# Optimization experiments

Measured on AMD Instinct MI355X. Metric: run time of the kernel, lower is better.

Reference implementation:

```python
import jax, jax.numpy as jnp
import numpy as np

B, CIN, COUT, T, H, W, NH = 8, 16, 16, 32, 16, 16, 4
DIN = CIN * H * W    # 4096
DOUT = COUT * H * W  # 4096
DH = DOUT // NH      # 1024


def conv3d(x, w, b, pad):
    y = jax.lax.conv_general_dilated(
        x, w, window_strides=(1, 1, 1), padding=((pad, pad),) * 3,
        dimension_numbers=('NCDHW', 'OIDHW', 'NCDHW'))
    return y + b[None, :, None, None, None]


def instance_norm(x, eps=1e-5):
    # InstanceNorm3d default: no affine, normalize per (B,C) over (T,H,W)
    mu = x.mean(axis=(2, 3, 4), keepdims=True)
    var = ((x - mu) ** 2).mean(axis=(2, 3, 4), keepdims=True)
    return (x - mu) * jax.lax.rsqrt(var + eps)


def slstm(x, Wg, bg, Rg):
    # x: (B,T,D). Wg: (4,D,D) input weights [i,f,z,o]; bg: (4,D);
    # Rg: (NH,4,DH,DH) block-diagonal per-head recurrent weights.
    Bb, Tt, D = x.shape
    Gx = jnp.einsum('btd,god->btgo', x, Wg) + bg  # (B,T,4,D)

    def step(carry, gx):
        h, c, n, m = carry
        hh = h.reshape(Bb, NH, DH)
        gh = jnp.einsum('bhd,hgod->bhgo', hh, Rg)          # (B,NH,4,DH)
        pre = gx + gh.transpose(0, 2, 1, 3).reshape(Bb, 4, D)
        i_pre, f_pre, z_pre, o_pre = pre[:, 0], pre[:, 1], pre[:, 2], pre[:, 3]
        # stabilized exponential gating (xLSTM sLSTM)
        m_new = jnp.maximum(f_pre + m, i_pre)
        i = jnp.exp(i_pre - m_new)
        f = jnp.exp(f_pre + m - m_new)
        c = f * c + i * jnp.tanh(z_pre)
        n = f * n + i
        h = jax.nn.sigmoid(o_pre) * c / n
        return (h, c, n, m_new), h

    init = tuple(jnp.zeros((Bb, D), x.dtype) for _ in range(4))
    _, hs = jax.lax.scan(step, init, Gx.transpose(1, 0, 2, 3))  # hs: (T,B,D)
    return hs.transpose(1, 0, 2)


def setup_inputs():
    key = jax.random.key(0)
    ks = jax.random.split(key, 8)
    s = 0.02
    return {
        'x': jax.random.normal(ks[0], (B, CIN, T, H, W), jnp.float32),
        'c1_w': jax.random.normal(ks[1], (COUT, CIN, 3, 3, 3), jnp.float32) * 0.05,
        'c1_b': jnp.zeros((COUT,), jnp.float32),
        'c2_w': jax.random.normal(ks[2], (COUT, COUT, 3, 3, 3), jnp.float32) * 0.05,
        'c2_b': jnp.zeros((COUT,), jnp.float32),
        'c3_w': jax.random.normal(ks[3], (COUT, COUT, 3, 3, 3), jnp.float32) * 0.05,
        'c3_b': jnp.zeros((COUT,), jnp.float32),
        'pre_w': jax.random.normal(ks[4], (DOUT, DIN), jnp.float32) * s,
        'pre_b': jnp.zeros((DOUT,), jnp.float32),
        'lstm_W': jax.random.normal(ks[5], (4, DOUT, DOUT), jnp.float32) * s,
        'lstm_b': jnp.zeros((4, DOUT), jnp.float32),
        'lstm_R': jax.random.normal(ks[6], (NH, 4, DH, DH), jnp.float32) * s,
        'attn_w': jax.random.normal(ks[7], (1, 2 * COUT), jnp.float32) * 0.05,
        'attn_b': jnp.zeros((1,), jnp.float32),
    }


def reference(x, c1_w, c1_b, c2_w, c2_b, c3_w, c3_b, pre_w, pre_b,
              lstm_W, lstm_b, lstm_R, attn_w, attn_b):
    # conv3d branch: conv -> IN -> relu -> conv -> relu -> conv -> relu
    y = jax.nn.relu(instance_norm(conv3d(x, c1_w, c1_b, 1)))
    y = jax.nn.relu(conv3d(y, c2_w, c2_b, 1))
    out3d = jax.nn.relu(conv3d(y, c3_w, c3_b, 1))
    # sLSTM branch
    xs = x.transpose(0, 2, 1, 3, 4).reshape(B, T, DIN)
    xs = xs @ pre_w.T + pre_b
    hs = slstm(xs, lstm_W, lstm_b, lstm_R)                 # (B,T,DOUT)
    s_out = hs.reshape(B, T, COUT, H, W).transpose(0, 2, 1, 3, 4)
    # attention-gated fusion: cat -> 1x1x1 conv -> sigmoid -> weighted sum
    comb = jnp.concatenate([s_out, out3d], axis=1)         # (B,2*COUT,T,H,W)
    alpha = jax.nn.sigmoid(jnp.einsum('bcthw,oc->bothw', comb, attn_w)
                           + attn_b[None, :, None, None, None])
    return alpha * out3d + (1 - alpha) * s_out
```

## Files before the change

### kernel.cpp

```cpp
#include <hip/hip_runtime.h>
#include <hip/hip_bf16.h>
#include <cstddef>

#define BB   8
#define CIN  16
#define COUT 16
#define TT   32
#define HH   16
#define WW   16
#define DIN  4096
#define DOUT 4096
#define NH   4
#define DH   1024
#define SPAT 8192
#define NSEQ 256

typedef __attribute__((ext_vector_type(8))) short  bf16x8;
typedef __attribute__((ext_vector_type(4))) float  f32x4;
typedef __attribute__((ext_vector_type(4))) unsigned short us4;
typedef unsigned short ushort_t;
typedef unsigned long long u64_t;

static __device__ __forceinline__ ushort_t f2bf(float f) {
    union { float f; unsigned u; } v; v.f = f;
    unsigned r = (v.u + 0x7fffu + ((v.u >> 16) & 1u)) >> 16;
    return (ushort_t)r;
}
static __device__ __forceinline__ float bf2f(ushort_t u) {
    union { unsigned u; float f; } v; v.u = ((unsigned)u) << 16;
    return v.f;
}

__global__ void pack_xt_kernel(const float* __restrict__ x, ushort_t* __restrict__ xt) {
    int idx = blockIdx.x * 256 + threadIdx.x;
    int n = idx >> 10, k4 = (idx & 1023) * 4;
    int b = n >> 5, t = n & 31, c = k4 >> 8, hw = k4 & 255;
    f32x4 f = *(const f32x4*)&x[(((size_t)(b * CIN + c) * TT + t)) * 256 + hw];
    us4 o;
    #pragma unroll
    for (int i = 0; i < 4; ++i) o[i] = f2bf(f[i]);
    *(us4*)&xt[(size_t)n * DIN + k4] = o;
}

__global__ void pack_cw_kernel(const float* __restrict__ w1, const float* __restrict__ w2,
                               const float* __restrict__ w3,
                               float* __restrict__ cw1, float* __restrict__ cw2,
                               float* __restrict__ cw3) {
    int i = blockIdx.x * 256 + threadIdx.x;
    int set = i / 6912, j = i - set * 6912;
    const float* w = (set == 0) ? w1 : (set == 1) ? w2 : w3;
    float* cw      = (set == 0) ? cw1 : (set == 1) ? cw2 : cw3;
    int o = j & 15, r = j >> 4;
    int k = r % 27, ci = r / 27;
    cw[j] = w[(size_t)(o * CIN + ci) * 27 + k];
}

template<int BN, bool OUT_BF16>
__global__ __launch_bounds__(256, 2)
void mfma_gemm_kernel(const ushort_t* __restrict__ A, const float* __restrict__ B,
                      const float* __restrict__ bias, void* __restrict__ C,
                      int N, int K) {
    constexpr int NF  = BN / 16;
    constexpr int TPR = 256 / BN;
    constexpr int FPT = 64 / TPR;
    __shared__ ushort_t Al[2][256][64];
    __shared__ ushort_t Bl[2][BN][64];
    int tid  = threadIdx.x;
    int lane = tid & 63;
    int wv   = tid >> 6;
    int n0 = blockIdx.x * BN;

    f32x4 acc[4][NF];
    #pragma unroll
    for (int i = 0; i < 4; ++i)
        #pragma unroll
        for (int j = 0; j < NF; ++j) acc[i][j] = (f32x4){0.f, 0.f, 0.f, 0.f};

    auto stageA = [&](int buf, int k0) {
        #pragma unroll
        for (int q = 0; q < 8; ++q) {
            int row = wv * 64 + q * 8 + (lane >> 3);
            const ushort_t* g = A + (size_t)row * K + k0 + (lane & 7) * 8;
            __builtin_amdgcn_global_load_lds(
                (const __attribute__((address_space(1))) void*)g,
                (__attribute__((address_space(3))) void*)&Al[buf][wv * 64 + q * 8][0],
                16, 0, 0);
        }
    };
    auto stageB = [&](int buf, int k0) {
        int r  = tid / TPR;
        int cs = (tid % TPR) * FPT;
        const float* g = B + (size_t)(n0 + r) * K + k0 + cs;
        #pragma unroll
        for (int q = 0; q < FPT / 4; ++q) {
            f32x4 f = *(const f32x4*)(g + q * 4);
            us4 pk;
            #pragma unroll
            for (int e = 0; e < 4; ++e) pk[e] = f2bf(f[e]);
            *(us4*)&Bl[buf][r][cs + q * 4] = pk;
        }
    };
    auto compute = [&](int buf) {
        #pragma unroll
        for (int ks = 0; ks < 2; ++ks) {
            bf16x8 af[4], bfr[NF];
            #pragma unroll
            for (int i = 0; i < 4; ++i)
                af[i] = *(const bf16x8*)&Al[buf][wv * 64 + i * 16 + (lane & 15)][ks * 32 + (lane >> 4) * 8];
            #pragma unroll
            for (int j = 0; j < NF; ++j)
                bfr[j] = *(const bf16x8*)&Bl[buf][j * 16 + (lane & 15)][ks * 32 + (lane >> 4) * 8];
            #pragma unroll
            for (int i = 0; i < 4; ++i)
                #pragma unroll
                for (int j = 0; j < NF; ++j)
                    acc[i][j] = __builtin_amdgcn_mfma_f32_16x16x32_bf16(af[i], bfr[j], acc[i][j], 0, 0, 0);
        }
    };

    stageA(0, 0); stageB(0, 0);
    __syncthreads();
    int nk = K / 64;
    int cur = 0;
    for (int t = 0; t < nk; ++t) {
        if (t + 1 < nk) { stageA(cur ^ 1, (t + 1) * 64); stageB(cur ^ 1, (t + 1) * 64); }
        compute(cur);
        __syncthreads();
        cur ^= 1;
    }

    #pragma unroll
    for (int i = 0; i < 4; ++i) {
        int row = wv * 64 + i * 16 + (lane >> 4) * 4;
        #pragma unroll
        for (int j = 0; j < NF; ++j) {
            int col = n0 + j * 16 + (lane & 15);
            float bv = bias[col];
            #pragma unroll
            for (int r = 0; r < 4; ++r) {
                float v = acc[i][j][r] + bv;
                if constexpr (OUT_BF16) ((ushort_t*)C)[(size_t)(row + r) * N + col] = f2bf(v);
                else                    ((float*)C)[(size_t)(row + r) * N + col] = v;
            }
        }
    }
}

__global__ __launch_bounds__(256, 1)
void lstm_persist_kernel(const float* __restrict__ R,
                         const float* __restrict__ Gx,
                         unsigned* __restrict__ hfr,
                         int* __restrict__ flags) {
    __shared__ ushort_t Rl[4][32][64 * 8];
    __shared__ float gh_p[4][4][16][8];

    int tid  = threadIdx.x;
    int lane = tid & 63;
    int w    = tid >> 6;
    int head = blockIdx.x >> 6;
    int oc   = blockIdx.x & 63;

    #pragma unroll 4
    for (int n = 0; n < 64; ++n) {
        int g = n >> 4, r = n & 15;
        const float* src = R + ((size_t)((head * 4 + g) * DH + oc * 16 + r)) * DH + tid * 4;
        f32x4 f = *(const f32x4*)src;
        int k0 = tid * 4;
        int ks = k0 >> 5;
        int kI = (k0 >> 3) & 3;
        int e8 = k0 & 7;
        union { ushort_t u[4]; u64_t q; } pk;
        #pragma unroll
        for (int e = 0; e < 4; ++e) pk.u[e] = f2bf(f[e]);
        *(u64_t*)&Rl[g][ks][((kI << 4) | r) * 8 + e8] = pk.q;
    }

    int arow = lane & 15;
    int part = arow >> 3;
    int bb   = arow & 7;
    int kseg = lane >> 4;

    int gb  = tid >> 4;
    int gol = tid & 15;
    int gd  = head * DH + oc * 16 + gol;
    int o_h = oc * 16 + gol;
    unsigned hslot = ((unsigned)head * 32 + (o_h >> 5)) * 256 + gb * 32 + (o_h & 31);
    float c_r = 0.f, n_r = 0.f, m_r = 0.f;

    __syncthreads();

    for (int t = 0; t < TT; ++t) {
        float gx0 = 0.f, gx1 = 0.f, gx2 = 0.f, gx3 = 0.f;
        if (tid < 128) {
            size_t gxoff = ((size_t)(gb * TT + t)) * (4 * DOUT) + gd;
            gx0 = Gx[gxoff];
            gx1 = Gx[gxoff + DOUT];
            gx2 = Gx[gxoff + 2 * DOUT];
            gx3 = Gx[gxoff + 3 * DOUT];
        }

        if (t > 0) {
            const int* fl = flags + (((t - 1) * 4 + head) << 6);
            for (;;) {
                int v = __hip_atomic_load(fl + lane, __ATOMIC_RELAXED,
                                          __HIP_MEMORY_SCOPE_AGENT);
                if (__all(v != 0)) break;
                __builtin_amdgcn_s_sleep(1);
            }

            const u64_t* hb = (const u64_t*)hfr
                + ((((size_t)(t - 1) * 4 + head) * 32) * 256 + bb * 32 + kseg * 8) / 2;
            bf16x8 hf[8];
            #pragma unroll
            for (int j = 0; j < 8; ++j) {
                const u64_t* p = hb + (size_t)(w * 8 + j) * 128;
                union { ushort_t u[8]; bf16x8 v; } fr;
                #pragma unroll
                for (int e2 = 0; e2 < 4; ++e2) {
                    u64_t q = __hip_atomic_load(p + e2, __ATOMIC_RELAXED,
                                                __HIP_MEMORY_SCOPE_AGENT);
                    unsigned q0 = (unsigned)q, q1 = (unsigned)(q >> 32);
                    fr.u[e2 * 2]     = part ? (ushort_t)(q0 >> 16) : (ushort_t)(q0 & 0xffffu);
                    fr.u[e2 * 2 + 1] = part ? (ushort_t)(q1 >> 16) : (ushort_t)(q1 & 0xffffu);
                }
                hf[j] = fr.v;
            }

            f32x4 acc[4];
            #pragma unroll
            for (int g = 0; g < 4; ++g) acc[g] = (f32x4){0.f, 0.f, 0.f, 0.f};
            #pragma unroll
            for (int g = 0; g < 4; ++g)
                #pragma unroll
                for (int j = 0; j < 8; ++j) {
                    bf16x8 a = *(const bf16x8*)&Rl[g][w * 8 + j][lane * 8];
                    acc[g] = __builtin_amdgcn_mfma_f32_16x16x32_bf16(a, hf[j], acc[g], 0, 0, 0);
                }
            #pragma unroll
            for (int g = 0; g < 4; ++g)
                #pragma unroll
                for (int r = 0; r < 4; ++r)
                    acc[g][r] += __shfl_xor(acc[g][r], 8, 64);
            if (part == 0) {
                int orow0 = kseg * 4;
                #pragma unroll
                for (int g = 0; g < 4; ++g)
                    #pragma unroll
                    for (int r = 0; r < 4; ++r)
                        gh_p[w][g][orow0 + r][bb] = acc[g][r];
            }
        } else {
            for (int i = tid; i < 4 * 4 * 16 * 8; i += 256)
                ((float*)gh_p)[i] = 0.f;
        }
        __syncthreads();

        if (tid < 128) {
            float ip = gx0 +
                gh_p[0][0][gol][gb] + gh_p[1][0][gol][gb] + gh_p[2][0][gol][gb] + gh_p[3][0][gol][gb];
            float fp = gx1 +
                gh_p[0][1][gol][gb] + gh_p[1][1][gol][gb] + gh_p[2][1][gol][gb] + gh_p[3][1][gol][gb];
            float zp = gx2 +
                gh_p[0][2][gol][gb] + gh_p[1][2][gol][gb] + gh_p[2][2][gol][gb] + gh_p[3][2][gol][gb];
            float op = gx3 +
                gh_p[0][3][gol][gb] + gh_p[1][3][gol][gb] + gh_p[2][3][gol][gb] + gh_p[3][3][gol][gb];
            float mn = fmaxf(fp + m_r, ip);
            float iv = __expf(ip - mn);
            float fv = __expf(fp + m_r - mn);
            float zc = fminf(fmaxf(zp, -9.f), 9.f);
            float th = 1.f - 2.f / (__expf(2.f * zc) + 1.f);
            c_r = fv * c_r + iv * th;
            n_r = fv * n_r + iv;
            float sig = 1.f / (1.f + __expf(-op));
            float hv = sig * c_r / n_r;
            m_r = mn;
            unsigned hi = f2bf(hv);
            unsigned lo = f2bf(hv - bf2f((ushort_t)hi));
            __hip_atomic_store(&hfr[(size_t)t * 32768 + hslot],
                               hi | (lo << 16),
                               __ATOMIC_RELAXED, __HIP_MEMORY_SCOPE_AGENT);
        }
        __syncthreads();
        if (tid == 0)
            __hip_atomic_store(&flags[((t * 4 + head) << 6) + oc], 1,
                               __ATOMIC_RELAXED, __HIP_MEMORY_SCOPE_AGENT);
    }
}

template<bool NORM>
__global__ __launch_bounds__(256)
void conv3d_kernel(const float* __restrict__ in, const float* __restrict__ cw,
                   const float* __restrict__ bias, const float* __restrict__ stats,
                   float* __restrict__ out, int relu) {
    __shared__ float xin[CIN][3][256];
    int blk = blockIdx.x;
    int b = blk >> 6, t = (blk >> 1) & 31, half = blk & 1;
    int tid = threadIdx.x;

    for (int i = tid; i < CIN * 3 * 256; i += 256) {
        int hw = i & 255, r = i >> 8;
        int kt = r % 3, ci = r / 3;
        int tt = t + kt - 1;
        float v = 0.f;
        if ((unsigned)tt < TT) {
            v = in[((size_t)(b * CIN + ci) * TT + tt) * 256 + hw];
            if constexpr (NORM) {
                float mu = stats[(b * CIN + ci) * 2];
                float rs = stats[(b * CIN + ci) * 2 + 1];
                v = fmaxf((v - mu) * rs, 0.f);
            }
        }
        xin[ci][kt][hw] = v;
    }
    __syncthreads();

    int h = tid >> 4, wx = tid & 15;
    f32x4 a0 = *(const f32x4*)&bias[half * 8];
    f32x4 a1 = *(const f32x4*)&bias[half * 8 + 4];

    for (int ci = 0; ci < CIN; ++ci) {
        #pragma unroll
        for (int kt = 0; kt < 3; ++kt) {
            #pragma unroll
            for (int kh = 0; kh < 3; ++kh) {
                int h2 = h + kh - 1;
                bool vh = (unsigned)h2 < HH;
                int h2c = vh ? h2 : 0;
                #pragma unroll
                for (int kw = 0; kw < 3; ++kw) {
                    int w2 = wx + kw - 1;
                    bool v = vh && ((unsigned)w2 < WW);
                    int w2c = ((unsigned)w2 < WW) ? w2 : 0;
                    float xv = xin[ci][kt][h2c * 16 + w2c];
                    xv = v ? xv : 0.f;
                    const float* wp = cw + (size_t)(ci * 27 + kt * 9 + kh * 3 + kw) * 16 + half * 8;
                    f32x4 w0 = *(const f32x4*)(wp);
                    f32x4 w1 = *(const f32x4*)(wp + 4);
                    a0 += xv * w0; a1 += xv * w1;
                }
            }
        }
    }
    float accs[8];
    #pragma unroll
    for (int i = 0; i < 4; ++i) { accs[i] = a0[i]; accs[4 + i] = a1[i]; }
    #pragma unroll
    for (int o = 0; o < 8; ++o) {
        float v = accs[o];
        if (relu) v = fmaxf(v, 0.f);
        out[((size_t)(b * COUT + half * 8 + o) * TT + t) * 256 + tid] = v;
    }
}

__global__ void inorm_stats_kernel(const float* __restrict__ y, float* __restrict__ stats) {
    __shared__ float s1[256], s2[256];
    const float* p = y + (size_t)blockIdx.x * SPAT;
    float sum = 0.f, sq = 0.f;
    for (int i = threadIdx.x; i < SPAT; i += 256) {
        float v = p[i];
        sum += v; sq += v * v;
    }
    s1[threadIdx.x] = sum; s2[threadIdx.x] = sq;
    __syncthreads();
    for (int s = 128; s > 0; s >>= 1) {
        if (threadIdx.x < s) { s1[threadIdx.x] += s1[threadIdx.x + s]; s2[threadIdx.x] += s2[threadIdx.x + s]; }
        __syncthreads();
    }
    if (threadIdx.x == 0) {
        float mu = s1[0] / (float)SPAT;
        float var = s2[0] / (float)SPAT - mu * mu;
        stats[blockIdx.x * 2]     = mu;
        stats[blockIdx.x * 2 + 1] = rsqrtf(var + 1e-5f);
    }
}

__global__ void combine_kernel(const unsigned* __restrict__ hfr,
                               const float* __restrict__ out3d,
                               const float* __restrict__ attn_w,
                               const float* __restrict__ attn_b,
                               float* __restrict__ out) {
    int idx = blockIdx.x * 256 + threadIdx.x;
    int hw = idx & 255;
    int t  = (idx >> 8) & 31;
    int b  = idx >> 13;
    float dot = attn_b[0];
    float sv[16], ov[16];
    #pragma unroll
    for (int ch = 0; ch < 16; ++ch) {
        int d = ch * 256 + hw;
        int head = d >> 10, o_h = d & 1023;
        size_t slot = (size_t)t * 32768 + (size_t)head * 8192
                    + (o_h >> 5) * 256 + b * 32 + (o_h & 31);
        unsigned v32 = hfr[slot];
        float s = bf2f((ushort_t)(v32 & 0xffffu)) + bf2f((ushort_t)(v32 >> 16));
        float o3 = out3d[(((size_t)(b * COUT + ch) * TT + t)) * 256 + hw];
        sv[ch] = s; ov[ch] = o3;
        dot += attn_w[ch] * s + attn_w[16 + ch] * o3;
    }
    float alpha = 1.f / (1.f + expf(-dot));
    #pragma unroll
    for (int ch = 0; ch < 16; ++ch) {
        out[(((size_t)(b * COUT + ch) * TT + t)) * 256 + hw] =
            alpha * ov[ch] + (1.f - alpha) * sv[ch];
    }
}

extern "C" void kernel_launch(void* const* d_in, const int* in_sizes, int n_in,
                              void* d_out, int out_size, void* d_ws, size_t ws_size,
                              hipStream_t stream) {
    const float* x      = (const float*)d_in[0];
    const float* c1_w   = (const float*)d_in[1];
    const float* c1_b   = (const float*)d_in[2];
    const float* c2_w   = (const float*)d_in[3];
    const float* c2_b   = (const float*)d_in[4];
    const float* c3_w   = (const float*)d_in[5];
    const float* c3_b   = (const float*)d_in[6];
    const float* pre_w  = (const float*)d_in[7];
    const float* pre_b  = (const float*)d_in[8];
    const float* lstm_W = (const float*)d_in[9];
    const float* lstm_b = (const float*)d_in[10];
    const float* lstm_R = (const float*)d_in[11];
    const float* attn_w = (const float*)d_in[12];
    const float* attn_b = (const float*)d_in[13];
    float* out = (float*)d_out;

    float* wsf = (float*)d_ws;
    float* y1    = wsf;
    float* y2    = y1 + 1048576;
    float* out3d = y2 + 1048576;
    float* Gx    = out3d + 1048576;
    float* cw1   = Gx + 4194304;
    float* cw2   = cw1 + 6912;
    float* cw3   = cw2 + 6912;
    float* stats = cw3 + 6912;
    float* pad   = stats + 256;
    ushort_t* xt   = (ushort_t*)(pad + 64);
    ushort_t* xs2b = xt + 1048576;
    unsigned* hfr  = (unsigned*)(xs2b + 1048576);
    int*     flags = (int*)(hfr + 1048576);

    hipMemsetAsync(flags, 0, 8192 * sizeof(int), stream);

    pack_xt_kernel<<<1024, 256, 0, stream>>>(x, xt);
    pack_cw_kernel<<<81, 256, 0, stream>>>(c1_w, c2_w, c3_w, cw1, cw2, cw3);

    conv3d_kernel<false><<<512, 256, 0, stream>>>(x, cw1, c1_b, nullptr, y1, 0);
    inorm_stats_kernel<<<128, 256, 0, stream>>>(y1, stats);
    conv3d_kernel<true><<<512, 256, 0, stream>>>(y1, cw2, c2_b, stats, y2, 1);
    conv3d_kernel<false><<<512, 256, 0, stream>>>(y2, cw3, c3_b, nullptr, out3d, 1);

    mfma_gemm_kernel<16, true><<<DOUT / 16, 256, 0, stream>>>(
        xt, pre_w, pre_b, xs2b, DOUT, DIN);
    mfma_gemm_kernel<32, false><<<4 * DOUT / 32, 256, 0, stream>>>(
        xs2b, lstm_W, lstm_b, Gx, 4 * DOUT, DOUT);

    lstm_persist_kernel<<<256, 256, 0, stream>>>(lstm_R, Gx, hfr, flags);

    combine_kernel<<<256, 256, 0, stream>>>(hfr, out3d, attn_w, attn_b, out);
}
```

Measured before the change: 590.2 us.

## Split-K the gate GEMM, fuse setup kernels, and fold instance-norm stats into conv

Merges the input pack, the conv-weight pack and the flag memset into one setup kernel. Computes the per-tile instance-norm partial sums inside the first conv's epilogue, so the stats kernel shrinks to one small block and y1 is not reread. Splits the large gate GEMM's K dimension in two over gridDim.y, writing two partial outputs that the LSTM kernel adds together along with the bias. This raises block count and parallelism for the big GEMM and cuts launches, at the cost of an extra 16MB partial buffer that is written and then read inside the serial recurrence loop.

```diff
diff --git a/kernel.cpp b/kernel.cpp
--- a/kernel.cpp
+++ b/kernel.cpp
@@ -18,6 +18,7 @@
 typedef __attribute__((ext_vector_type(8))) short  bf16x8;
 typedef __attribute__((ext_vector_type(4))) float  f32x4;
 typedef __attribute__((ext_vector_type(4))) unsigned short us4;
+typedef __attribute__((ext_vector_type(4))) int    i32x4;
 typedef unsigned short ushort_t;
 typedef unsigned long long u64_t;
 
@@ -31,31 +32,38 @@
     return v.f;
 }
 
-__global__ void pack_xt_kernel(const float* __restrict__ x, ushort_t* __restrict__ xt) {
-    int idx = blockIdx.x * 256 + threadIdx.x;
-    int n = idx >> 10, k4 = (idx & 1023) * 4;
-    int b = n >> 5, t = n & 31, c = k4 >> 8, hw = k4 & 255;
-    f32x4 f = *(const f32x4*)&x[(((size_t)(b * CIN + c) * TT + t)) * 256 + hw];
-    us4 o;
-    #pragma unroll
-    for (int i = 0; i < 4; ++i) o[i] = f2bf(f[i]);
-    *(us4*)&xt[(size_t)n * DIN + k4] = o;
-}
-
-__global__ void pack_cw_kernel(const float* __restrict__ w1, const float* __restrict__ w2,
-                               const float* __restrict__ w3,
-                               float* __restrict__ cw1, float* __restrict__ cw2,
-                               float* __restrict__ cw3) {
-    int i = blockIdx.x * 256 + threadIdx.x;
-    int set = i / 6912, j = i - set * 6912;
-    const float* w = (set == 0) ? w1 : (set == 1) ? w2 : w3;
-    float* cw      = (set == 0) ? cw1 : (set == 1) ? cw2 : cw3;
-    int o = j & 15, r = j >> 4;
-    int k = r % 27, ci = r / 27;
-    cw[j] = w[(size_t)(o * CIN + ci) * 27 + k];
-}
-
-template<int BN, bool OUT_BF16>
+__global__ void setup_kernel(const float* __restrict__ x, ushort_t* __restrict__ xt,
+                             const float* __restrict__ w1, const float* __restrict__ w2,
+                             const float* __restrict__ w3,
+                             float* __restrict__ cw1, float* __restrict__ cw2,
+                             float* __restrict__ cw3, int* __restrict__ flags) {
+    int bid = blockIdx.x;
+    if (bid < 1024) {
+        int idx = bid * 256 + threadIdx.x;
+        int n = idx >> 10, k4 = (idx & 1023) * 4;
+        int b = n >> 5, t = n & 31, c = k4 >> 8, hw = k4 & 255;
+        f32x4 f = *(const f32x4*)&x[(((size_t)(b * CIN + c) * TT + t)) * 256 + hw];
+        us4 o;
+        #pragma unroll
+        for (int i = 0; i < 4; ++i) o[i] = f2bf(f[i]);
+        *(us4*)&xt[(size_t)n * DIN + k4] = o;
+    } else if (bid < 1105) {
+        int i = (bid - 1024) * 256 + threadIdx.x;
+        if (i < 3 * 6912) {
+            int set = i / 6912, j = i - set * 6912;
+            const float* w = (set == 0) ? w1 : (set == 1) ? w2 : w3;
+            float* cw      = (set == 0) ? cw1 : (set == 1) ? cw2 : cw3;
+            int o = j & 15, r = j >> 4;
+            int k = r % 27, ci = r / 27;
+            cw[j] = w[(size_t)(o * CIN + ci) * 27 + k];
+        }
+    } else {
+        int j = (bid - 1105) * 256 + threadIdx.x;
+        ((i32x4*)flags)[j] = (i32x4){0, 0, 0, 0};
+    }
+}
+
+template<int BN, bool OUT_BF16, bool ADD_BIAS>
 __global__ __launch_bounds__(256, 2)
 void mfma_gemm_kernel(const ushort_t* __restrict__ A, const float* __restrict__ B,
                       const float* __restrict__ bias, void* __restrict__ C,
@@ -69,6 +77,8 @@
     int lane = tid & 63;
     int wv   = tid >> 6;
     int n0 = blockIdx.x * BN;
+    int ksp = K / gridDim.y;
+    int kS  = blockIdx.y * ksp;
 
     f32x4 acc[4][NF];
     #pragma unroll
@@ -118,29 +128,30 @@
         }
     };
 
-    stageA(0, 0); stageB(0, 0);
+    stageA(0, kS); stageB(0, kS);
     __syncthreads();
-    int nk = K / 64;
+    int nk = ksp / 64;
     int cur = 0;
     for (int t = 0; t < nk; ++t) {
-        if (t + 1 < nk) { stageA(cur ^ 1, (t + 1) * 64); stageB(cur ^ 1, (t + 1) * 64); }
+        if (t + 1 < nk) { stageA(cur ^ 1, kS + (t + 1) * 64); stageB(cur ^ 1, kS + (t + 1) * 64); }
         compute(cur);
         __syncthreads();
         cur ^= 1;
     }
 
+    size_t cofs = (size_t)blockIdx.y * 256 * N;
     #pragma unroll
     for (int i = 0; i < 4; ++i) {
         int row = wv * 64 + i * 16 + (lane >> 4) * 4;
         #pragma unroll
         for (int j = 0; j < NF; ++j) {
             int col = n0 + j * 16 + (lane & 15);
-            float bv = bias[col];
+            float bv = ADD_BIAS ? bias[col] : 0.f;
             #pragma unroll
             for (int r = 0; r < 4; ++r) {
                 float v = acc[i][j][r] + bv;
-                if constexpr (OUT_BF16) ((ushort_t*)C)[(size_t)(row + r) * N + col] = f2bf(v);
-                else                    ((float*)C)[(size_t)(row + r) * N + col] = v;
+                if constexpr (OUT_BF16) ((ushort_t*)C)[cofs + (size_t)(row + r) * N + col] = f2bf(v);
+                else                    ((float*)C)[cofs + (size_t)(row + r) * N + col] = v;
             }
         }
     }
@@ -148,7 +159,9 @@
 
 __global__ __launch_bounds__(256, 1)
 void lstm_persist_kernel(const float* __restrict__ R,
-                         const float* __restrict__ Gx,
+                         const float* __restrict__ GxA,
+                         const float* __restrict__ GxB,
+                         const float* __restrict__ lstm_b,
                          unsigned* __restrict__ hfr,
                          int* __restrict__ flags) {
     __shared__ ushort_t Rl[4][32][64 * 8];
@@ -186,6 +199,13 @@
     int o_h = oc * 16 + gol;
     unsigned hslot = ((unsigned)head * 32 + (o_h >> 5)) * 256 + gb * 32 + (o_h & 31);
     float c_r = 0.f, n_r = 0.f, m_r = 0.f;
+    float lb0 = 0.f, lb1 = 0.f, lb2 = 0.f, lb3 = 0.f;
+    if (tid < 128) {
+        lb0 = lstm_b[gd];
+        lb1 = lstm_b[DOUT + gd];
+        lb2 = lstm_b[2 * DOUT + gd];
+        lb3 = lstm_b[3 * DOUT + gd];
+    }
 
     __syncthreads();
 
@@ -193,10 +213,10 @@
         float gx0 = 0.f, gx1 = 0.f, gx2 = 0.f, gx3 = 0.f;
         if (tid < 128) {
             size_t gxoff = ((size_t)(gb * TT + t)) * (4 * DOUT) + gd;
-            gx0 = Gx[gxoff];
-            gx1 = Gx[gxoff + DOUT];
-            gx2 = Gx[gxoff + 2 * DOUT];
-            gx3 = Gx[gxoff + 3 * DOUT];
+            gx0 = GxA[gxoff]            + GxB[gxoff]            + lb0;
+            gx1 = GxA[gxoff + DOUT]     + GxB[gxoff + DOUT]     + lb1;
+            gx2 = GxA[gxoff + 2 * DOUT] + GxB[gxoff + 2 * DOUT] + lb2;
+            gx3 = GxA[gxoff + 3 * DOUT] + GxB[gxoff + 3 * DOUT] + lb3;
         }
 
         if (t > 0) {
@@ -287,11 +307,11 @@
     }
 }
 
-template<bool NORM>
+template<bool NORM, bool PSUM>
 __global__ __launch_bounds__(256)
 void conv3d_kernel(const float* __restrict__ in, const float* __restrict__ cw,
                    const float* __restrict__ bias, const float* __restrict__ stats,
-                   float* __restrict__ out, int relu) {
+                   float* __restrict__ out, float* __restrict__ psum, int relu) {
     __shared__ float xin[CIN][3][256];
     int blk = blockIdx.x;
     int b = blk >> 6, t = (blk >> 1) & 31, half = blk & 1;
@@ -350,27 +370,47 @@
         if (relu) v = fmaxf(v, 0.f);
         out[((size_t)(b * COUT + half * 8 + o) * TT + t) * 256 + tid] = v;
     }
-}
-
-__global__ void inorm_stats_kernel(const float* __restrict__ y, float* __restrict__ stats) {
-    __shared__ float s1[256], s2[256];
-    const float* p = y + (size_t)blockIdx.x * SPAT;
-    float sum = 0.f, sq = 0.f;
-    for (int i = threadIdx.x; i < SPAT; i += 256) {
-        float v = p[i];
-        sum += v; sq += v * v;
-    }
-    s1[threadIdx.x] = sum; s2[threadIdx.x] = sq;
-    __syncthreads();
-    for (int s = 128; s > 0; s >>= 1) {
-        if (threadIdx.x < s) { s1[threadIdx.x] += s1[threadIdx.x + s]; s2[threadIdx.x] += s2[threadIdx.x + s]; }
+
+    if constexpr (PSUM) {
         __syncthreads();
-    }
-    if (threadIdx.x == 0) {
-        float mu = s1[0] / (float)SPAT;
-        float var = s2[0] / (float)SPAT - mu * mu;
-        stats[blockIdx.x * 2]     = mu;
-        stats[blockIdx.x * 2 + 1] = rsqrtf(var + 1e-5f);
+        float* sm = (float*)xin;
+        int wv = tid >> 6;
+        #pragma unroll
+        for (int o = 0; o < 8; ++o) {
+            float s = accs[o];
+            float q = accs[o] * accs[o];
+            #pragma unroll
+            for (int m = 1; m < 64; m <<= 1) {
+                s += __shfl_xor(s, m, 64);
+                q += __shfl_xor(q, m, 64);
+            }
+            if ((tid & 63) == 0) { sm[wv * 16 + o * 2] = s; sm[wv * 16 + o * 2 + 1] = q; }
+        }
+        __syncthreads();
+        if (tid < 16) {
+            int o = tid >> 1, which = tid & 1;
+            float v = sm[o * 2 + which] + sm[16 + o * 2 + which]
+                    + sm[32 + o * 2 + which] + sm[48 + o * 2 + which];
+            psum[((((size_t)(b * 32 + t) * 2 + half) * 8 + o) * 2) + which] = v;
+        }
+    }
+}
+
+__global__ void inorm_stats_kernel(const float* __restrict__ psum, float* __restrict__ stats) {
+    int tid = threadIdx.x;
+    if (tid < 128) {
+        int b = tid >> 4, c = tid & 15;
+        int half = c >> 3, ch = c & 7;
+        float sum = 0.f, sq = 0.f;
+        for (int t = 0; t < TT; ++t) {
+            size_t base = (((size_t)(b * 32 + t) * 2 + half) * 8 + ch) * 2;
+            sum += psum[base];
+            sq  += psum[base + 1];
+        }
+        float mu = sum / (float)SPAT;
+        float var = sq / (float)SPAT - mu * mu;
+        stats[(b * CIN + c) * 2]     = mu;
+        stats[(b * CIN + c) * 2 + 1] = rsqrtf(var + 1e-5f);
     }
 }
 
@@ -428,33 +468,32 @@
     float* y1    = wsf;
     float* y2    = y1 + 1048576;
     float* out3d = y2 + 1048576;
-    float* Gx    = out3d + 1048576;
-    float* cw1   = Gx + 4194304;
+    float* GxA   = out3d + 1048576;
+    float* GxB   = GxA + 4194304;
+    float* cw1   = GxB + 4194304;
     float* cw2   = cw1 + 6912;
     float* cw3   = cw2 + 6912;
     float* stats = cw3 + 6912;
-    float* pad   = stats + 256;
+    float* psum  = stats + 256;
+    float* pad   = psum + 8192;
     ushort_t* xt   = (ushort_t*)(pad + 64);
     ushort_t* xs2b = xt + 1048576;
     unsigned* hfr  = (unsigned*)(xs2b + 1048576);
     int*     flags = (int*)(hfr + 1048576);
 
-    hipMemsetAsync(flags, 0, 8192 * sizeof(int), stream);
-
-    pack_xt_kernel<<<1024, 256, 0, stream>>>(x, xt);
-    pack_cw_kernel<<<81, 256, 0, stream>>>(c1_w, c2_w, c3_w, cw1, cw2, cw3);
-
-    conv3d_kernel<false><<<512, 256, 0, stream>>>(x, cw1, c1_b, nullptr, y1, 0);
-    inorm_stats_kernel<<<128, 256, 0, stream>>>(y1, stats);
-    conv3d_kernel<true><<<512, 256, 0, stream>>>(y1, cw2, c2_b, stats, y2, 1);
-    conv3d_kernel<false><<<512, 256, 0, stream>>>(y2, cw3, c3_b, nullptr, out3d, 1);
-
-    mfma_gemm_kernel<16, true><<<DOUT / 16, 256, 0, stream>>>(
+    setup_kernel<<<1113, 256, 0, stream>>>(x, xt, c1_w, c2_w, c3_w, cw1, cw2, cw3, flags);
+
+    conv3d_kernel<false, true><<<512, 256, 0, stream>>>(x, cw1, c1_b, nullptr, y1, psum, 0);
+    inorm_stats_kernel<<<1, 256, 0, stream>>>(psum, stats);
+    conv3d_kernel<true, false><<<512, 256, 0, stream>>>(y1, cw2, c2_b, stats, y2, nullptr, 1);
+    conv3d_kernel<false, false><<<512, 256, 0, stream>>>(y2, cw3, c3_b, nullptr, out3d, nullptr, 1);
+
+    mfma_gemm_kernel<16, true, true><<<dim3(DOUT / 16, 1), 256, 0, stream>>>(
         xt, pre_w, pre_b, xs2b, DOUT, DIN);
-    mfma_gemm_kernel<32, false><<<4 * DOUT / 32, 256, 0, stream>>>(
-        xs2b, lstm_W, lstm_b, Gx, 4 * DOUT, DOUT);
-
-    lstm_persist_kernel<<<256, 256, 0, stream>>>(lstm_R, Gx, hfr, flags);
+    mfma_gemm_kernel<32, false, false><<<dim3(4 * DOUT / 32, 2), 256, 0, stream>>>(
+        xs2b, lstm_W, nullptr, GxA, 4 * DOUT, DOUT);
+
+    lstm_persist_kernel<<<256, 256, 0, stream>>>(lstm_R, GxA, GxB, lstm_b, hfr, flags);
 
     combine_kernel<<<256, 256, 0, stream>>>(hfr, out3d, attn_w, attn_b, out);
 }
```

Measured after the change: 586.5 us. Within noise of the previous version (-0.6%).
